# Performance work log

Hardware: AMD Instinct MI355X
Metric: run time of the kernel (lower is better)

The kernel has to match this reference:

```python
import jax, jax.numpy as jnp
import numpy as np

HEADS = 8
DIM_HEAD = 64
SCALE = DIM_HEAD ** -0.5


def setup_inputs() -> dict:
    key = jax.random.key(0)
    ks = jax.random.split(key, 7)
    b, p, n, dim = 4, 8, 512, 512
    inner = HEADS * DIM_HEAD
    std = dim ** -0.5
    return {
        "q_in": jax.random.normal(ks[0], (b, p, n, dim), jnp.float32),
        "kv_in": jax.random.normal(ks[1], (b, p, n, dim), jnp.float32),
        "Wq": jax.random.normal(ks[2], (dim, inner), jnp.float32) * std,
        "Wk": jax.random.normal(ks[3], (dim, inner), jnp.float32) * std,
        "Wv": jax.random.normal(ks[4], (dim, inner), jnp.float32) * std,
        "Wo": jax.random.normal(ks[5], (inner, dim), jnp.float32) * std,
        "bo": jnp.zeros((dim,), jnp.float32),
    }


def _split_heads(x):
    # [b, p, n, h*d] -> [b, h, p, n, d]
    b, p, n, hd = x.shape
    return x.reshape(b, p, n, HEADS, DIM_HEAD).transpose(0, 3, 1, 2, 4)


def reference(q_in, kv_in, Wq, Wk, Wv, Wo, bo):
    q = _split_heads(q_in @ Wq)
    k = _split_heads(kv_in @ Wk)
    v = _split_heads(kv_in @ Wv)
    dots = jnp.einsum('bhpid,bhpjd->bhpij', q, k) * SCALE
    attn = jax.nn.softmax(dots, axis=-1)
    out = jnp.einsum('bhpij,bhpjd->bhpid', attn, v)
    # [b, h, p, n, d] -> [b, p, n, h*d]
    b, h, p, n, d = out.shape
    out = out.transpose(0, 2, 3, 1, 4).reshape(b, p, n, h * d)
    return out @ Wo + bo
```

## Files before the change

kernel.cpp:

```cpp
#include <hip/hip_runtime.h>

typedef unsigned short u16;
typedef unsigned int   u32;
typedef u16  u16x8 __attribute__((ext_vector_type(8)));
typedef u16  u16x4 __attribute__((ext_vector_type(4)));
typedef float f32x4 __attribute__((ext_vector_type(4)));
typedef __bf16 bf16x8 __attribute__((ext_vector_type(8)));

#define SEQ   512
#define DIM   512
#define DHEAD 64
#define M_ROWS 16384

#define AS1 __attribute__((address_space(1)))
#define AS3 __attribute__((address_space(3)))
#define GLL16(gp, lp) __builtin_amdgcn_global_load_lds((const AS1 void*)(gp), (AS3 void*)(lp), 16, 0, 0)

#define WAIT_VM_BAR(LIT) do { asm volatile("s_waitcnt vmcnt(" LIT ")" ::: "memory"); __builtin_amdgcn_s_barrier(); } while (0)
#define LGKM_BAR()       do { asm volatile("s_waitcnt lgkmcnt(0)" ::: "memory"); __builtin_amdgcn_s_barrier(); } while (0)

__device__ __forceinline__ u16 f2b(float f) {
  u32 x = __builtin_bit_cast(u32, f);
  return (u16)((x + 0x7fffu + ((x >> 16) & 1u)) >> 16);
}

__global__ __launch_bounds__(256) void prep(const float* __restrict__ q,
                                            const float* __restrict__ kv,
                                            const float* __restrict__ Wq,
                                            const float* __restrict__ Wk,
                                            const float* __restrict__ Wv,
                                            const float* __restrict__ Wo,
                                            u16* __restrict__ qb,
                                            u16* __restrict__ kvb,
                                            u16* __restrict__ wout) {
  __shared__ float tile[32][33];
  const int bid = blockIdx.x;
  if (bid < 8192) {
    const float* src = (bid >= 4096) ? kv : q;
    u16* dst = (bid >= 4096) ? kvb : qb;
    size_t i = ((size_t)(bid & 4095) * 256 + threadIdx.x) * 8;
    float4 a = *reinterpret_cast<const float4*>(&src[i]);
    float4 b = *reinterpret_cast<const float4*>(&src[i + 4]);
    u16x8 o;
    o[0] = f2b(a.x); o[1] = f2b(a.y); o[2] = f2b(a.z); o[3] = f2b(a.w);
    o[4] = f2b(b.x); o[5] = f2b(b.y); o[6] = f2b(b.z); o[7] = f2b(b.w);
    *reinterpret_cast<u16x8*>(&dst[i]) = o;
  } else {
    const int rem = bid - 8192;
    const int z = rem >> 8;
    const int t = rem & 255;
    const int n0 = (t & 15) * 32;
    const int k0 = (t >> 4) * 32;
    const int tid = threadIdx.x;
    const int tx = tid & 31, ty = tid >> 5;
    const float* W = (z == 0) ? Wq : (z == 1) ? Wk : (z == 2) ? Wv : Wo;
#pragma unroll
    for (int i = 0; i < 4; i++) {
      int r = ty + i * 8;
      tile[r][tx] = W[(k0 + r) * DIM + n0 + tx];
    }
    __syncthreads();
    u16* o = wout + (size_t)z * DIM * DIM;
#pragma unroll
    for (int i = 0; i < 4; i++) {
      int r = ty + i * 8;
      o[(n0 + r) * DIM + k0 + tx] = f2b(tile[tx][r]);
    }
  }
}

__global__ __launch_bounds__(256, 2) void gemm_qkv(const u16* __restrict__ Qin,
                                                   const u16* __restrict__ KVin,
                                                   const u16* __restrict__ Wqt,
                                                   const u16* __restrict__ Wkt,
                                                   const u16* __restrict__ Wvt,
                                                   u16* __restrict__ Qb,
                                                   u16* __restrict__ Kb,
                                                   u16* __restrict__ Vt) {
  __shared__ __attribute__((aligned(16))) u16 As[2][128 * 32];
  __shared__ __attribute__((aligned(16))) u16 Bs[2][128 * 32];
  const int tid = threadIdx.x;
  const int lane = tid & 63;
  const int w = tid >> 6;
  const int l15 = lane & 15;
  const int quad = lane >> 4;
  const int z = blockIdx.z;
  const int d = blockIdx.x;
  const int bid = (d & 7) * 64 + (d >> 3);
  const int wr = (w >> 1) * 64, wc = (w & 1) * 64;
  const int srow = lane >> 2;
  const int scol = (lane & 3) * 8;

  int gm, gn;
  const u16 *A, *B;
  if (z < 2) {
    gm = (bid >> 2) * 128;  gn = (bid & 3) * 128;
    A = z ? KVin : Qin;  B = z ? Wkt : Wqt;
  } else {
    gm = (bid & 3) * 128;   gn = (bid >> 2) * 128;
    A = Wvt; B = KVin;
  }

  f32x4 acc[4][4] = {};

  auto stage = [&](int kk, int b) {
    const int k0 = kk * 32;
#pragma unroll
    for (int i = 0; i < 2; i++) {
      int r0 = w * 32 + i * 16;
      GLL16(&A[(size_t)(gm + r0 + srow) * DIM + k0 + scol], &As[b][r0 * 32]);
      GLL16(&B[(size_t)(gn + r0 + srow) * DIM + k0 + scol], &Bs[b][r0 * 32]);
    }
  };

  stage(0, 0);
  for (int kk = 0; kk < 16; kk++) {
    const int cur = kk & 1;
    if (kk < 15) {
      stage(kk + 1, cur ^ 1);
      WAIT_VM_BAR("4");
    } else {
      WAIT_VM_BAR("0");
    }

    bf16x8 af[4], bfr[4];
#pragma unroll
    for (int mt = 0; mt < 4; mt++)
      af[mt] = *reinterpret_cast<const bf16x8*>(&As[cur][(wr + mt * 16 + l15) * 32 + quad * 8]);
#pragma unroll
    for (int nt = 0; nt < 4; nt++)
      bfr[nt] = *reinterpret_cast<const bf16x8*>(&Bs[cur][(wc + nt * 16 + l15) * 32 + quad * 8]);
#pragma unroll
    for (int mt = 0; mt < 4; mt++)
#pragma unroll
      for (int nt = 0; nt < 4; nt++)
        acc[mt][nt] = __builtin_amdgcn_mfma_f32_16x16x32_bf16(af[mt], bfr[nt], acc[mt][nt], 0, 0, 0);

    LGKM_BAR();
  }

  if (z < 2) {
    u16* C = (z == 0) ? Qb : Kb;
#pragma unroll
    for (int mt = 0; mt < 4; mt++)
#pragma unroll
      for (int nt = 0; nt < 4; nt++)
#pragma unroll
        for (int r = 0; r < 4; r++)
          C[(size_t)(gm + wr + mt * 16 + quad * 4 + r) * DIM + gn + wc + nt * 16 + l15] = f2b(acc[mt][nt][r]);
  } else {
#pragma unroll
    for (int mt = 0; mt < 4; mt++)
#pragma unroll
      for (int nt = 0; nt < 4; nt++)
#pragma unroll
        for (int r = 0; r < 4; r++)
          Vt[(size_t)(gm + wr + mt * 16 + quad * 4 + r) * M_ROWS + gn + wc + nt * 16 + l15] = f2b(acc[mt][nt][r]);
  }
}

__global__ __launch_bounds__(256) void attn(const u16* __restrict__ Qb,
                                            const u16* __restrict__ Kb,
                                            const u16* __restrict__ Vtg,
                                            u16* __restrict__ Ob) {
  __shared__ __attribute__((aligned(16))) u16 Ks[2 * 64 * 32];
  __shared__ __attribute__((aligned(16))) u16 Vs[2 * 64 * 32];
  __shared__ __attribute__((aligned(16))) u16 Pq[4][2][16 * 72];

  const int tid = threadIdx.x;
  const int lane = tid & 63;
  const int w = tid >> 6;
  const int l15 = lane & 15;
  const int quad = lane >> 4;
  const int srow = lane >> 2;
  const int scol = (lane & 3) * 8;

  const int d = blockIdx.x;
  const int bid = (d & 7) * 128 + (d >> 3);
  const int qt = bid & 3;
  const int bhp = bid >> 2;
  const int h = bhp & 7;
  const int bp = bhp >> 3;
  const int qrow0 = bp * SEQ + qt * 128;
  const int col0 = h * DHEAD;

  const float SCL = 0.18033688011112042f;

  bf16x8 qf[2][2];
#pragma unroll
  for (int g = 0; g < 2; g++)
#pragma unroll
    for (int kd = 0; kd < 2; kd++)
      qf[g][kd] = *reinterpret_cast<const bf16x8*>(
          &Qb[(size_t)(qrow0 + w * 32 + g * 16 + l15) * DIM + col0 + kd * 32 + quad * 8]);

  float l_[2] = {0.0f, 0.0f};
  f32x4 o[2][4] = {};

  for (int j = 0; j < 8; j++) {
    __syncthreads();
    const int krow0 = bp * SEQ + j * 64;
#pragma unroll
    for (int i = 0; i < 2; i++) {
      int t = w * 2 + i;
      int plane = t & 1, chunk = t >> 1;
      GLL16(&Kb[(size_t)(krow0 + chunk * 16 + srow) * DIM + col0 + plane * 32 + scol],
            &Ks[plane * 2048 + chunk * 512]);
    }
#pragma unroll
    for (int i = 0; i < 2; i++) {
      int t = w * 2 + i;
      int plane = t & 1, chunk = t >> 1;
      GLL16(&Vtg[(size_t)(col0 + chunk * 16 + srow) * M_ROWS + krow0 + plane * 32 + scol],
            &Vs[plane * 2048 + chunk * 512]);
    }
    __syncthreads();

#pragma unroll
    for (int g = 0; g < 2; g++) {
      f32x4 st[4];
#pragma unroll
      for (int ct = 0; ct < 4; ct++) {
        f32x4 z = {};
#pragma unroll
        for (int kd = 0; kd < 2; kd++) {
          bf16x8 kf = *reinterpret_cast<const bf16x8*>(&Ks[kd * 2048 + (ct * 16 + l15) * 32 + quad * 8]);
          z = __builtin_amdgcn_mfma_f32_16x16x32_bf16(kf, qf[g][kd], z, 0, 0, 0);
        }
        st[ct] = z * SCL;
      }

      float rs = 0.0f;
#pragma unroll
      for (int ct = 0; ct < 4; ct++)
#pragma unroll
        for (int r = 0; r < 4; r++) {
          float pv = __builtin_amdgcn_exp2f(st[ct][r]);
          st[ct][r] = pv;
          rs += pv;
        }
      rs += __shfl_xor(rs, 16);
      rs += __shfl_xor(rs, 32);
      l_[g] += rs;

#pragma unroll
      for (int ct = 0; ct < 4; ct++) {
        u16x4 pk;
#pragma unroll
        for (int e = 0; e < 4; e++) pk[e] = f2b(st[ct][e]);
        *reinterpret_cast<u16x4*>(&Pq[w][g][l15 * 72 + ct * 16 + quad * 4]) = pk;
      }

#pragma unroll
      for (int c2 = 0; c2 < 2; c2++) {
        bf16x8 af = *reinterpret_cast<const bf16x8*>(&Pq[w][g][l15 * 72 + c2 * 32 + quad * 8]);
#pragma unroll
        for (int nt = 0; nt < 4; nt++) {
          bf16x8 bv = *reinterpret_cast<const bf16x8*>(&Vs[c2 * 2048 + (nt * 16 + l15) * 32 + quad * 8]);
          o[g][nt] = __builtin_amdgcn_mfma_f32_16x16x32_bf16(af, bv, o[g][nt], 0, 0, 0);
        }
      }
    }
  }

#pragma unroll
  for (int g = 0; g < 2; g++) {
    float inv = 1.0f / l_[g];
#pragma unroll
    for (int r = 0; r < 4; r++) {
      float lr = __shfl(inv, quad * 4 + r);
      int row = qrow0 + w * 32 + g * 16 + quad * 4 + r;
#pragma unroll
      for (int nt = 0; nt < 4; nt++)
        Ob[(size_t)row * DIM + col0 + nt * 16 + l15] = f2b(o[g][nt][r] * lr);
    }
  }
}

__global__ __launch_bounds__(256) void gemm_out(const u16* __restrict__ Ab,
                                                const u16* __restrict__ Bt,
                                                const float* __restrict__ bias,
                                                float* __restrict__ C) {
  __shared__ __attribute__((aligned(16))) u16 As[2][128 * 32];
  __shared__ __attribute__((aligned(16))) u16 Bs[2][128 * 32];
  const int tid = threadIdx.x;
  const int lane = tid & 63;
  const int w = tid >> 6;
  const int l15 = lane & 15;
  const int quad = lane >> 4;
  const int d = blockIdx.x;
  const int bid = (d & 7) * 64 + (d >> 3);
  const int gn = (bid & 3) * 128;
  const int gm = (bid >> 2) * 128;
  const int wr = (w >> 1) * 64, wc = (w & 1) * 64;
  const int srow = lane >> 2;
  const int scol = (lane & 3) * 8;

  f32x4 acc[4][4] = {};

  auto stage = [&](int kk, int b) {
    const int k0 = kk * 32;
#pragma unroll
    for (int i = 0; i < 2; i++) {
      int r0 = w * 32 + i * 16;
      GLL16(&Ab[(size_t)(gm + r0 + srow) * DIM + k0 + scol], &As[b][r0 * 32]);
      GLL16(&Bt[(size_t)(gn + r0 + srow) * DIM + k0 + scol], &Bs[b][r0 * 32]);
    }
  };

  stage(0, 0);
  for (int kk = 0; kk < 16; kk++) {
    const int cur = kk & 1;
    if (kk < 15) {
      stage(kk + 1, cur ^ 1);
      WAIT_VM_BAR("4");
    } else {
      WAIT_VM_BAR("0");
    }

    bf16x8 af[4], bfr[4];
#pragma unroll
    for (int mt = 0; mt < 4; mt++)
      af[mt] = *reinterpret_cast<const bf16x8*>(&As[cur][(wr + mt * 16 + l15) * 32 + quad * 8]);
#pragma unroll
    for (int nt = 0; nt < 4; nt++)
      bfr[nt] = *reinterpret_cast<const bf16x8*>(&Bs[cur][(wc + nt * 16 + l15) * 32 + quad * 8]);
#pragma unroll
    for (int mt = 0; mt < 4; mt++)
#pragma unroll
      for (int nt = 0; nt < 4; nt++)
        acc[mt][nt] = __builtin_amdgcn_mfma_f32_16x16x32_bf16(af[mt], bfr[nt], acc[mt][nt], 0, 0, 0);

    LGKM_BAR();
  }

#pragma unroll
  for (int mt = 0; mt < 4; mt++)
#pragma unroll
    for (int nt = 0; nt < 4; nt++) {
      float bcol = bias[gn + wc + nt * 16 + l15];
#pragma unroll
      for (int r = 0; r < 4; r++)
        C[(size_t)(gm + wr + mt * 16 + quad * 4 + r) * DIM + gn + wc + nt * 16 + l15] = acc[mt][nt][r] + bcol;
    }
}

extern "C" void kernel_launch(void* const* d_in, const int* in_sizes, int n_in,
                              void* d_out, int out_size, void* d_ws, size_t ws_size,
                              hipStream_t stream) {
  const float* q_in  = (const float*)d_in[0];
  const float* kv_in = (const float*)d_in[1];
  const float* Wq    = (const float*)d_in[2];
  const float* Wk    = (const float*)d_in[3];
  const float* Wv    = (const float*)d_in[4];
  const float* Wo    = (const float*)d_in[5];
  const float* bo    = (const float*)d_in[6];
  float* out = (float*)d_out;

  u16* ws = (u16*)d_ws;
  u16* Wqt = ws;
  u16* Wkt = ws + 262144;
  u16* Wvt = ws + 524288;
  u16* Wot = ws + 786432;
  u16* Qb  = ws + 1048576;
  u16* Kb  = Qb + (size_t)M_ROWS * DIM;
  u16* Vtg = Kb + (size_t)M_ROWS * DIM;
  u16* Ob  = Vtg + (size_t)M_ROWS * DIM;
  u16* Qin_b  = (u16*)d_out;
  u16* KVin_b = Qin_b + (size_t)M_ROWS * DIM;

  prep<<<dim3(9216), 256, 0, stream>>>(q_in, kv_in, Wq, Wk, Wv, Wo, Qin_b, KVin_b, ws);
  gemm_qkv<<<dim3(512, 1, 3), 256, 0, stream>>>(Qin_b, KVin_b, Wqt, Wkt, Wvt, Qb, Kb, Vtg);
  attn<<<dim3(1024), 256, 0, stream>>>(Qb, Kb, Vtg, Ob);
  gemm_out<<<dim3(512), 256, 0, stream>>>(Ob, Wot, bo, out);
}
```

Baseline: 199.5 us.

## Fuse fp32-to-bf16 input conversion into QKV GEMM, drop LDS staging

Removes the separate pass that converted q_in and kv_in to bf16 in the prep kernel. The QKV GEMM now reads the fp32 activations and converts them in registers. The same GEMM also drops its double-buffered LDS staging and loads MFMA fragments directly from global memory. This saves a full read and write of both activation tensors. In exchange there is no LDS reuse across waves, and each block re-reads its fp32 A or B data from global or cache with twice the bytes.

```diff
diff --git a/kernel.cpp b/kernel.cpp
--- a/kernel.cpp
+++ b/kernel.cpp
@@ -24,61 +24,49 @@
   return (u16)((x + 0x7fffu + ((x >> 16) & 1u)) >> 16);
 }
 
-__global__ __launch_bounds__(256) void prep(const float* __restrict__ q,
-                                            const float* __restrict__ kv,
-                                            const float* __restrict__ Wq,
+__device__ __forceinline__ bf16x8 cvt8(float4 a, float4 b) {
+  bf16x8 r;
+  r[0] = (__bf16)a.x; r[1] = (__bf16)a.y; r[2] = (__bf16)a.z; r[3] = (__bf16)a.w;
+  r[4] = (__bf16)b.x; r[5] = (__bf16)b.y; r[6] = (__bf16)b.z; r[7] = (__bf16)b.w;
+  return r;
+}
+
+__global__ __launch_bounds__(256) void prep(const float* __restrict__ Wq,
                                             const float* __restrict__ Wk,
                                             const float* __restrict__ Wv,
                                             const float* __restrict__ Wo,
-                                            u16* __restrict__ qb,
-                                            u16* __restrict__ kvb,
                                             u16* __restrict__ wout) {
   __shared__ float tile[32][33];
   const int bid = blockIdx.x;
-  if (bid < 8192) {
-    const float* src = (bid >= 4096) ? kv : q;
-    u16* dst = (bid >= 4096) ? kvb : qb;
-    size_t i = ((size_t)(bid & 4095) * 256 + threadIdx.x) * 8;
-    float4 a = *reinterpret_cast<const float4*>(&src[i]);
-    float4 b = *reinterpret_cast<const float4*>(&src[i + 4]);
-    u16x8 o;
-    o[0] = f2b(a.x); o[1] = f2b(a.y); o[2] = f2b(a.z); o[3] = f2b(a.w);
-    o[4] = f2b(b.x); o[5] = f2b(b.y); o[6] = f2b(b.z); o[7] = f2b(b.w);
-    *reinterpret_cast<u16x8*>(&dst[i]) = o;
-  } else {
-    const int rem = bid - 8192;
-    const int z = rem >> 8;
-    const int t = rem & 255;
-    const int n0 = (t & 15) * 32;
-    const int k0 = (t >> 4) * 32;
-    const int tid = threadIdx.x;
-    const int tx = tid & 31, ty = tid >> 5;
-    const float* W = (z == 0) ? Wq : (z == 1) ? Wk : (z == 2) ? Wv : Wo;
-#pragma unroll
-    for (int i = 0; i < 4; i++) {
-      int r = ty + i * 8;
-      tile[r][tx] = W[(k0 + r) * DIM + n0 + tx];
-    }
-    __syncthreads();
-    u16* o = wout + (size_t)z * DIM * DIM;
-#pragma unroll
-    for (int i = 0; i < 4; i++) {
-      int r = ty + i * 8;
-      o[(n0 + r) * DIM + k0 + tx] = f2b(tile[tx][r]);
-    }
-  }
-}
-
-__global__ __launch_bounds__(256, 2) void gemm_qkv(const u16* __restrict__ Qin,
-                                                   const u16* __restrict__ KVin,
+  const int z = bid >> 8;
+  const int t = bid & 255;
+  const int n0 = (t & 15) * 32;
+  const int k0 = (t >> 4) * 32;
+  const int tid = threadIdx.x;
+  const int tx = tid & 31, ty = tid >> 5;
+  const float* W = (z == 0) ? Wq : (z == 1) ? Wk : (z == 2) ? Wv : Wo;
+#pragma unroll
+  for (int i = 0; i < 4; i++) {
+    int r = ty + i * 8;
+    tile[r][tx] = W[(k0 + r) * DIM + n0 + tx];
+  }
+  __syncthreads();
+  u16* o = wout + (size_t)z * DIM * DIM;
+#pragma unroll
+  for (int i = 0; i < 4; i++) {
+    int r = ty + i * 8;
+    o[(n0 + r) * DIM + k0 + tx] = f2b(tile[tx][r]);
+  }
+}
+
+__global__ __launch_bounds__(256, 2) void gemm_qkv(const float* __restrict__ Qin,
+                                                   const float* __restrict__ KVin,
                                                    const u16* __restrict__ Wqt,
                                                    const u16* __restrict__ Wkt,
                                                    const u16* __restrict__ Wvt,
                                                    u16* __restrict__ Qb,
                                                    u16* __restrict__ Kb,
                                                    u16* __restrict__ Vt) {
-  __shared__ __attribute__((aligned(16))) u16 As[2][128 * 32];
-  __shared__ __attribute__((aligned(16))) u16 Bs[2][128 * 32];
   const int tid = threadIdx.x;
   const int lane = tid & 63;
   const int w = tid >> 6;
@@ -88,58 +76,33 @@
   const int d = blockIdx.x;
   const int bid = (d & 7) * 64 + (d >> 3);
   const int wr = (w >> 1) * 64, wc = (w & 1) * 64;
-  const int srow = lane >> 2;
-  const int scol = (lane & 3) * 8;
-
-  int gm, gn;
-  const u16 *A, *B;
+
+  f32x4 acc[4][4] = {};
+
   if (z < 2) {
-    gm = (bid >> 2) * 128;  gn = (bid & 3) * 128;
-    A = z ? KVin : Qin;  B = z ? Wkt : Wqt;
-  } else {
-    gm = (bid & 3) * 128;   gn = (bid >> 2) * 128;
-    A = Wvt; B = KVin;
-  }
-
-  f32x4 acc[4][4] = {};
-
-  auto stage = [&](int kk, int b) {
-    const int k0 = kk * 32;
-#pragma unroll
-    for (int i = 0; i < 2; i++) {
-      int r0 = w * 32 + i * 16;
-      GLL16(&A[(size_t)(gm + r0 + srow) * DIM + k0 + scol], &As[b][r0 * 32]);
-      GLL16(&B[(size_t)(gn + r0 + srow) * DIM + k0 + scol], &Bs[b][r0 * 32]);
-    }
-  };
-
-  stage(0, 0);
-  for (int kk = 0; kk < 16; kk++) {
-    const int cur = kk & 1;
-    if (kk < 15) {
-      stage(kk + 1, cur ^ 1);
-      WAIT_VM_BAR("4");
-    } else {
-      WAIT_VM_BAR("0");
-    }
-
-    bf16x8 af[4], bfr[4];
-#pragma unroll
-    for (int mt = 0; mt < 4; mt++)
-      af[mt] = *reinterpret_cast<const bf16x8*>(&As[cur][(wr + mt * 16 + l15) * 32 + quad * 8]);
-#pragma unroll
-    for (int nt = 0; nt < 4; nt++)
-      bfr[nt] = *reinterpret_cast<const bf16x8*>(&Bs[cur][(wc + nt * 16 + l15) * 32 + quad * 8]);
-#pragma unroll
-    for (int mt = 0; mt < 4; mt++)
-#pragma unroll
-      for (int nt = 0; nt < 4; nt++)
-        acc[mt][nt] = __builtin_amdgcn_mfma_f32_16x16x32_bf16(af[mt], bfr[nt], acc[mt][nt], 0, 0, 0);
-
-    LGKM_BAR();
-  }
-
-  if (z < 2) {
+    const float* A = z ? KVin : Qin;
+    const u16*   B = z ? Wkt : Wqt;
+    const int gm = (bid >> 2) * 128;
+    const int gn = (bid & 3) * 128;
+#pragma unroll 2
+    for (int k0 = 0; k0 < DIM; k0 += 32) {
+      bf16x8 af[4], bfr[4];
+#pragma unroll
+      for (int mt = 0; mt < 4; mt++) {
+        const float* ap = &A[(size_t)(gm + wr + mt * 16 + l15) * DIM + k0 + quad * 8];
+        float4 x = *reinterpret_cast<const float4*>(ap);
+        float4 y = *reinterpret_cast<const float4*>(ap + 4);
+        af[mt] = cvt8(x, y);
+      }
+#pragma unroll
+      for (int nt = 0; nt < 4; nt++)
+        bfr[nt] = *reinterpret_cast<const bf16x8*>(&B[(size_t)(gn + wc + nt * 16 + l15) * DIM + k0 + quad * 8]);
+#pragma unroll
+      for (int mt = 0; mt < 4; mt++)
+#pragma unroll
+        for (int nt = 0; nt < 4; nt++)
+          acc[mt][nt] = __builtin_amdgcn_mfma_f32_16x16x32_bf16(af[mt], bfr[nt], acc[mt][nt], 0, 0, 0);
+    }
     u16* C = (z == 0) ? Qb : Kb;
 #pragma unroll
     for (int mt = 0; mt < 4; mt++)
@@ -149,6 +112,27 @@
         for (int r = 0; r < 4; r++)
           C[(size_t)(gm + wr + mt * 16 + quad * 4 + r) * DIM + gn + wc + nt * 16 + l15] = f2b(acc[mt][nt][r]);
   } else {
+    const int gm = (bid & 3) * 128;
+    const int gn = (bid >> 2) * 128;
+#pragma unroll 2
+    for (int k0 = 0; k0 < DIM; k0 += 32) {
+      bf16x8 af[4], bfr[4];
+#pragma unroll
+      for (int mt = 0; mt < 4; mt++)
+        af[mt] = *reinterpret_cast<const bf16x8*>(&Wvt[(size_t)(gm + wr + mt * 16 + l15) * DIM + k0 + quad * 8]);
+#pragma unroll
+      for (int nt = 0; nt < 4; nt++) {
+        const float* bp = &KVin[(size_t)(gn + wc + nt * 16 + l15) * DIM + k0 + quad * 8];
+        float4 x = *reinterpret_cast<const float4*>(bp);
+        float4 y = *reinterpret_cast<const float4*>(bp + 4);
+        bfr[nt] = cvt8(x, y);
+      }
+#pragma unroll
+      for (int mt = 0; mt < 4; mt++)
+#pragma unroll
+        for (int nt = 0; nt < 4; nt++)
+          acc[mt][nt] = __builtin_amdgcn_mfma_f32_16x16x32_bf16(af[mt], bfr[nt], acc[mt][nt], 0, 0, 0);
+    }
 #pragma unroll
     for (int mt = 0; mt < 4; mt++)
 #pragma unroll
@@ -366,11 +350,9 @@
   u16* Kb  = Qb + (size_t)M_ROWS * DIM;
   u16* Vtg = Kb + (size_t)M_ROWS * DIM;
   u16* Ob  = Vtg + (size_t)M_ROWS * DIM;
-  u16* Qin_b  = (u16*)d_out;
-  u16* KVin_b = Qin_b + (size_t)M_ROWS * DIM;
-
-  prep<<<dim3(9216), 256, 0, stream>>>(q_in, kv_in, Wq, Wk, Wv, Wo, Qin_b, KVin_b, ws);
-  gemm_qkv<<<dim3(512, 1, 3), 256, 0, stream>>>(Qin_b, KVin_b, Wqt, Wkt, Wvt, Qb, Kb, Vtg);
+
+  prep<<<dim3(1024), 256, 0, stream>>>(Wq, Wk, Wv, Wo, ws);
+  gemm_qkv<<<dim3(512, 1, 3), 256, 0, stream>>>(q_in, kv_in, Wqt, Wkt, Wvt, Qb, Kb, Vtg);
   attn<<<dim3(1024), 256, 0, stream>>>(Qb, Kb, Vtg, Ob);
   gemm_out<<<dim3(512), 256, 0, stream>>>(Ob, Wot, bo, out);
 }
```

Result: slower. 290.5 us (+45.6%).
